# Performance work log

Hardware: AMD Instinct MI355X
Metric: run time of the kernel (lower is better)

The kernel has to match this reference:

```python
import jax, jax.numpy as jnp
import numpy as np

WIN = 11          # win_size
NC = 2            # num_classes
SMOOTH = 0.1      # smoothing / (num_classes - 1) = 0.1/1; fix_flag=True and 0.1 <= Max_Smootning=0.2


def setup_inputs() -> dict:
    key = jax.random.key(0)
    k1, k2 = jax.random.split(key)
    x = jax.random.normal(k1, (8, 2, 1024, 1024), dtype=jnp.float32)
    target = jax.random.randint(k2, (8, 1, 1024, 1024), 0, 2, dtype=jnp.int32)
    return {"x": x, "target": target}


def reference(x, target):
    kern = -jnp.ones((1, 1, WIN, WIN), dtype=jnp.float32)
    kern = kern.at[0, 0, WIN // 2, WIN // 2].set(float(WIN * WIN - 1))

    tf = target.astype(jnp.float32)  # [B,1,H,W]
    pad = WIN // 2
    edge = jax.lax.conv_general_dilated(tf, kern, window_strides=(1, 1),
                                        padding=[(pad, pad), (pad, pad)])
    edge = jnp.where(edge != 0, 1.0, 0.0)  # [B,1,H,W], 1 near label edges

    log_p = jax.nn.log_softmax(x, axis=1)  # [B,C,H,W]

    # One-hot masks (to_categorical with alpha=0 and alpha=smoothing).
    oh = jax.nn.one_hot(target[:, 0], NC, dtype=jnp.float32)  # [B,H,W,C]
    oh = jnp.transpose(oh, (0, 3, 1, 2))                      # [B,C,H,W]
    # alpha everywhere, 1 - alpha + alpha/NC at the true class
    soft = SMOOTH + oh * (1.0 - 2.0 * SMOOTH + SMOOTH / NC)

    mask = oh * (1.0 - edge) + soft * edge  # hard label off-edge, smoothed on-edge
    loss = jnp.mean(jnp.sum(mask * log_p, axis=1))
    return -loss
```

## Files before the change

kernel.cpp:

```cpp
#include <hip/hip_runtime.h>

#define HH 1024
#define WW 1024
#define BB 8
#define WORDS_X 16

typedef unsigned long long u64;

__global__ __launch_bounds__(256) void ls_pack(const int* __restrict__ tgt,
                                               u64* __restrict__ bits) {
    const int lane = threadIdx.x & 63;
    const size_t wv = ((size_t)blockIdx.x * 256 + threadIdx.x) >> 6;
    const size_t wbase = wv * 8;
    const int* p = tgt + wbase * 64 + lane;

    int v[8];
#pragma unroll
    for (int j = 0; j < 8; ++j) v[j] = p[j * 64];

    u64 mine = 0;
#pragma unroll
    for (int j = 0; j < 8; ++j) {
        u64 m = __ballot(v[j] != 0);
        if (lane == j) mine = m;
    }
    if (lane < 8) bits[wbase + lane] = mine;
}

__global__ __launch_bounds__(256) void ls_edge(const u64* __restrict__ bits,
                                               u64* __restrict__ ebits) {
    __shared__ u64 s_b[26][17], s_oh[26][17], s_ah[26][17];
    const int tid  = threadIdx.x;
    const int slab = blockIdx.x;
    const int b    = blockIdx.y;
    const int y0   = slab << 4;

#pragma unroll
    for (int i = tid; i < 416; i += 256) {
        int r = i >> 4, k = i & 15;
        int gy = y0 - 5 + r;
        u64 v = 0;
        if ((unsigned)gy < HH) v = bits[((size_t)(b << 10) + gy) * WORDS_X + k];
        s_b[r][k] = v;
    }
    __syncthreads();

#pragma unroll
    for (int i = tid; i < 416; i += 256) {
        int r = i >> 4, k = i & 15;
        u64 wm = s_b[r][k];
        u64 wl = k ? s_b[r][k - 1] : 0;
        u64 wr = (k < 15) ? s_b[r][k + 1] : 0;
        u64 oh = wm, ah = wm;
#pragma unroll
        for (int d = 1; d <= 5; ++d) {
            u64 vr = (wm >> d) | (wr << (64 - d));
            u64 vl = (wm << d) | (wl >> (64 - d));
            oh |= vr | vl;
            ah &= vr & vl;
        }
        s_oh[r][k] = oh;
        s_ah[r][k] = ah;
    }
    __syncthreads();

    {
        int r = tid >> 4, k = tid & 15;
        u64 ov = 0, av = ~0ULL;
#pragma unroll
        for (int j = 0; j < 11; ++j) { ov |= s_oh[r + j][k]; av &= s_ah[r + j][k]; }
        u64 tc = s_b[r + 5][k];
        ebits[((size_t)(b << 10) + y0 + r) * WORDS_X + k] = (ov & ~tc) | (~av & tc);
    }
}

__global__ __launch_bounds__(256) void ls_loss2(const float* __restrict__ x,
                                                const u64* __restrict__ bits,
                                                const u64* __restrict__ ebits,
                                                float* __restrict__ partial) {
    __shared__ float s_red[4];
    const int tid = threadIdx.x;
    const int b  = blockIdx.z;
    const int ty = blockIdx.y * 64;
    const int wx = blockIdx.x;

    const float* xb0 = x + ((size_t)b * 2) * HH * WW + (size_t)ty * WW + (wx << 6);
    const float* xb1 = xb0 + (size_t)HH * WW;
    const u64* tw = bits  + ((size_t)(b << 10) + ty) * WORDS_X + wx;
    const u64* ew = ebits + ((size_t)(b << 10) + ty) * WORDS_X + wx;

    const int r0 = tid >> 4;
    const int c4 = tid & 15;
    const int sh = c4 << 2;

    float4 v0[4], v1[4];
    u64 twv[4], ewv[4];
#pragma unroll
    for (int q = 0; q < 4; ++q) {
        const size_t r = (size_t)(r0 + (q << 4));
        v0[q] = ((const float4*)(xb0 + r * WW))[c4];
        v1[q] = ((const float4*)(xb1 + r * WW))[c4];
        twv[q] = tw[r * WORDS_X];
        ewv[q] = ew[r * WORDS_X];
    }

    float acc = 0.f;
#pragma unroll
    for (int q = 0; q < 4; ++q) {
        const unsigned t4 = (unsigned)(twv[q] >> sh) & 0xfu;
        const unsigned e4 = (unsigned)(ewv[q] >> sh) & 0xfu;
        const float* f0 = (const float*)&v0[q];
        const float* f1 = (const float*)&v1[q];
#pragma unroll
        for (int j = 0; j < 4; ++j) {
            int t = (t4 >> j) & 1;
            int e = (e4 >> j) & 1;
            float a0 = f0[j], a1 = f1[j];
            float m   = fmaxf(a0, a1);
            float lse = m + __logf(1.0f + __expf(-fabsf(a0 - a1)));
            float lp0 = a0 - lse, lp1 = a1 - lse;
            float lpt = t ? lp1 : lp0;
            float lpo = t ? lp0 : lp1;
            acc += e ? (0.95f * lpt + 0.1f * lpo) : lpt;
        }
    }

#pragma unroll
    for (int off = 32; off > 0; off >>= 1) acc += __shfl_down(acc, off, 64);
    if ((tid & 63) == 0) s_red[tid >> 6] = acc;
    __syncthreads();
    if (tid == 0) {
        int bid = (blockIdx.z * gridDim.y + blockIdx.y) * gridDim.x + blockIdx.x;
        partial[bid] = s_red[0] + s_red[1] + s_red[2] + s_red[3];
    }
}

__global__ __launch_bounds__(1024) void ls_final(const float* __restrict__ partial,
                                                 float* __restrict__ out) {
    __shared__ double s_red[16];
    const int tid = threadIdx.x;
    double s = (double)partial[tid] + (double)partial[tid + 1024];
#pragma unroll
    for (int off = 32; off > 0; off >>= 1) s += __shfl_down(s, off, 64);
    if ((tid & 63) == 0) s_red[tid >> 6] = s;
    __syncthreads();
    if (tid == 0) {
        double total = 0.0;
#pragma unroll
        for (int i = 0; i < 16; ++i) total += s_red[i];
        out[0] = (float)(-total * (1.0 / (8.0 * 1024.0 * 1024.0)));
    }
}

extern "C" void kernel_launch(void* const* d_in, const int* in_sizes, int n_in,
                              void* d_out, int out_size, void* d_ws, size_t ws_size,
                              hipStream_t stream) {
    const float* x  = (const float*)d_in[0];
    const int* tgt  = (const int*)d_in[1];

    float* partial = (float*)d_ws;
    u64* bits  = (u64*)((char*)d_ws + (16 << 10));
    u64* ebits = (u64*)((char*)d_ws + (16 << 10) + (1 << 20));

    hipLaunchKernelGGL(ls_pack, dim3(4096), dim3(256), 0, stream, tgt, bits);
    hipLaunchKernelGGL(ls_edge, dim3(64, 8), dim3(256), 0, stream, bits, ebits);
    hipLaunchKernelGGL(ls_loss2, dim3(16, 16, 8), dim3(256), 0, stream,
                       x, bits, ebits, partial);
    hipLaunchKernelGGL(ls_final, dim3(1), dim3(1024), 0, stream, partial, (float*)d_out);
}
```

Baseline: 121.7 us.

## Process one full row per block in loss kernel with nontemporal loads

The loss kernel now assigns one image row (1024 pixels, both channels) to each block, giving 8192 blocks where each thread handles 4 pixels. Previously each block covered a 64x64 tile with 16 pixels per thread. Loads of x are fully contiguous per block and use nontemporal hints to avoid cache pollution. The change gives more blocks with less work per thread, trading per-thread memory-level parallelism for more occupancy. The final reduction now sums 8192 partials, and the workspace offsets are enlarged to fit them.

```diff
diff --git a/kernel.cpp b/kernel.cpp
--- a/kernel.cpp
+++ b/kernel.cpp
@@ -6,6 +6,7 @@
 #define WORDS_X 16
 
 typedef unsigned long long u64;
+typedef float f4 __attribute__((ext_vector_type(4)));
 
 __global__ __launch_bounds__(256) void ls_pack(const int* __restrict__ tgt,
                                                u64* __restrict__ bits) {
@@ -74,72 +75,56 @@
     }
 }
 
-__global__ __launch_bounds__(256) void ls_loss2(const float* __restrict__ x,
+__global__ __launch_bounds__(256) void ls_loss3(const float* __restrict__ x,
                                                 const u64* __restrict__ bits,
                                                 const u64* __restrict__ ebits,
                                                 float* __restrict__ partial) {
     __shared__ float s_red[4];
     const int tid = threadIdx.x;
-    const int b  = blockIdx.z;
-    const int ty = blockIdx.y * 64;
-    const int wx = blockIdx.x;
+    const int R   = blockIdx.x;
+    const int b   = R >> 10;
+    const int y   = R & 1023;
 
-    const float* xb0 = x + ((size_t)b * 2) * HH * WW + (size_t)ty * WW + (wx << 6);
-    const float* xb1 = xb0 + (size_t)HH * WW;
-    const u64* tw = bits  + ((size_t)(b << 10) + ty) * WORDS_X + wx;
-    const u64* ew = ebits + ((size_t)(b << 10) + ty) * WORDS_X + wx;
+    const float* xr0 = x + ((size_t)b * 2) * (size_t)(HH * WW) + (size_t)y * WW;
+    const f4 v0 = __builtin_nontemporal_load(((const f4*)xr0) + tid);
+    const f4 v1 = __builtin_nontemporal_load(((const f4*)(xr0 + (size_t)HH * WW)) + tid);
 
-    const int r0 = tid >> 4;
-    const int c4 = tid & 15;
-    const int sh = c4 << 2;
-
-    float4 v0[4], v1[4];
-    u64 twv[4], ewv[4];
-#pragma unroll
-    for (int q = 0; q < 4; ++q) {
-        const size_t r = (size_t)(r0 + (q << 4));
-        v0[q] = ((const float4*)(xb0 + r * WW))[c4];
-        v1[q] = ((const float4*)(xb1 + r * WW))[c4];
-        twv[q] = tw[r * WORDS_X];
-        ewv[q] = ew[r * WORDS_X];
-    }
+    const size_t mrow = (size_t)R * WORDS_X + (tid >> 4);
+    const u64 tw = bits[mrow];
+    const u64 ew = ebits[mrow];
+    const int sh = (tid & 15) << 2;
+    const unsigned t4 = (unsigned)(tw >> sh) & 0xfu;
+    const unsigned e4 = (unsigned)(ew >> sh) & 0xfu;
 
     float acc = 0.f;
 #pragma unroll
-    for (int q = 0; q < 4; ++q) {
-        const unsigned t4 = (unsigned)(twv[q] >> sh) & 0xfu;
-        const unsigned e4 = (unsigned)(ewv[q] >> sh) & 0xfu;
-        const float* f0 = (const float*)&v0[q];
-        const float* f1 = (const float*)&v1[q];
-#pragma unroll
-        for (int j = 0; j < 4; ++j) {
-            int t = (t4 >> j) & 1;
-            int e = (e4 >> j) & 1;
-            float a0 = f0[j], a1 = f1[j];
-            float m   = fmaxf(a0, a1);
-            float lse = m + __logf(1.0f + __expf(-fabsf(a0 - a1)));
-            float lp0 = a0 - lse, lp1 = a1 - lse;
-            float lpt = t ? lp1 : lp0;
-            float lpo = t ? lp0 : lp1;
-            acc += e ? (0.95f * lpt + 0.1f * lpo) : lpt;
-        }
+    for (int j = 0; j < 4; ++j) {
+        int t = (t4 >> j) & 1;
+        int e = (e4 >> j) & 1;
+        float a0 = v0[j], a1 = v1[j];
+        float m   = fmaxf(a0, a1);
+        float lse = m + __logf(1.0f + __expf(-fabsf(a0 - a1)));
+        float lp0 = a0 - lse, lp1 = a1 - lse;
+        float lpt = t ? lp1 : lp0;
+        float lpo = t ? lp0 : lp1;
+        acc += e ? (0.95f * lpt + 0.1f * lpo) : lpt;
     }
 
 #pragma unroll
     for (int off = 32; off > 0; off >>= 1) acc += __shfl_down(acc, off, 64);
     if ((tid & 63) == 0) s_red[tid >> 6] = acc;
     __syncthreads();
-    if (tid == 0) {
-        int bid = (blockIdx.z * gridDim.y + blockIdx.y) * gridDim.x + blockIdx.x;
-        partial[bid] = s_red[0] + s_red[1] + s_red[2] + s_red[3];
-    }
+    if (tid == 0)
+        partial[R] = s_red[0] + s_red[1] + s_red[2] + s_red[3];
 }
 
 __global__ __launch_bounds__(1024) void ls_final(const float* __restrict__ partial,
                                                  float* __restrict__ out) {
     __shared__ double s_red[16];
     const int tid = threadIdx.x;
-    double s = (double)partial[tid] + (double)partial[tid + 1024];
+    double s = 0.0;
+#pragma unroll
+    for (int k = 0; k < 8; ++k) s += (double)partial[tid + (k << 10)];
 #pragma unroll
     for (int off = 32; off > 0; off >>= 1) s += __shfl_down(s, off, 64);
     if ((tid & 63) == 0) s_red[tid >> 6] = s;
@@ -159,12 +144,11 @@
     const int* tgt  = (const int*)d_in[1];
 
     float* partial = (float*)d_ws;
-    u64* bits  = (u64*)((char*)d_ws + (16 << 10));
-    u64* ebits = (u64*)((char*)d_ws + (16 << 10) + (1 << 20));
+    u64* bits  = (u64*)((char*)d_ws + (64 << 10));
+    u64* ebits = (u64*)((char*)d_ws + (64 << 10) + (1 << 20));
 
     hipLaunchKernelGGL(ls_pack, dim3(4096), dim3(256), 0, stream, tgt, bits);
     hipLaunchKernelGGL(ls_edge, dim3(64, 8), dim3(256), 0, stream, bits, ebits);
-    hipLaunchKernelGGL(ls_loss2, dim3(16, 16, 8), dim3(256), 0, stream,
-                       x, bits, ebits, partial);
+    hipLaunchKernelGGL(ls_loss3, dim3(8192), dim3(256), 0, stream, x, bits, ebits, partial);
     hipLaunchKernelGGL(ls_final, dim3(1), dim3(1024), 0, stream, partial, (float*)d_out);
 }
```

After: 122.1 us. Within noise of the previous version (+0.3%).
